# Kernel optimization log

Measured on AMD Instinct MI355X. Metric: run time of the kernel, lower is better.

The kernel has to match this reference:

```python
import jax, jax.numpy as jnp
import numpy as np

M, N, K, C, H = 100000, 8192, 32, 256, 8
DH = C // H
FF = 512
R = (15, 15, 7)  # 2*MAXRANGE-1 per axis for MAXRANGE=[8,8,4]


def _layer_norm(x, g, b, eps=1e-5):
    mu = jnp.mean(x, axis=-1, keepdims=True)
    xc = x - mu
    var = jnp.mean(xc * xc, axis=-1, keepdims=True)
    return xc * jax.lax.rsqrt(var + eps) * g + b


def setup_inputs() -> dict:
    key = jax.random.key(0)
    ks = iter(jax.random.split(key, 40))
    d = {}
    d['voxel_features'] = jax.random.normal(next(ks), (M, C), jnp.float32)
    d['query_coords'] = jax.random.normal(next(ks), (N, 3), jnp.float32)
    d['query_indices'] = jax.random.randint(next(ks), (N,), 0, M)
    d['gather_indices'] = jax.random.randint(next(ks), (N, K), 0, M)
    d['gather_mask'] = jax.random.randint(next(ks), (N, K), 0, 2).astype(bool)
    d['rel_x'] = jax.random.randint(next(ks), (N, K), 0, R[0])
    d['rel_y'] = jax.random.randint(next(ks), (N, K), 0, R[1])
    d['rel_z'] = jax.random.randint(next(ks), (N, K), 0, R[2])
    s = 0.02
    # pos_proj: Conv1d(3, C, 1) == linear on coords
    d['w_pos'] = jax.random.normal(next(ks), (3, C), jnp.float32) * s
    d['b_pos'] = jnp.zeros((C,), jnp.float32)
    for nm in ['q', 'k', 'v', 'proj']:
        d['w_' + nm] = jax.random.normal(next(ks), (C, C), jnp.float32) * (C ** -0.5)
        d['b_' + nm] = jnp.zeros((C,), jnp.float32)
    d['ln1_g'] = jnp.ones((C,), jnp.float32); d['ln1_b'] = jnp.zeros((C,), jnp.float32)
    d['ln2_g'] = jnp.ones((C,), jnp.float32); d['ln2_b'] = jnp.zeros((C,), jnp.float32)
    d['w_ff1'] = jax.random.normal(next(ks), (C, FF), jnp.float32) * (C ** -0.5)
    d['b_ff1'] = jnp.zeros((FF,), jnp.float32)
    d['w_ff2'] = jax.random.normal(next(ks), (FF, C), jnp.float32) * (FF ** -0.5)
    d['b_ff2'] = jnp.zeros((C,), jnp.float32)
    # per-axis relative position tables: [H, DH, 2W-1] for q-side and k-side
    for m in ['q', 'k']:
        for ax, r in zip(['x', 'y', 'z'], R):
            d[f'pos_{m}{ax}'] = jax.random.normal(next(ks), (H, DH, r), jnp.float32) * s
    return d


def reference(voxel_features, query_coords, query_indices, gather_indices, gather_mask,
              rel_x, rel_y, rel_z,
              w_pos, b_pos, w_q, b_q, w_k, b_k, w_v, b_v, w_proj, b_proj,
              ln1_g, ln1_b, ln2_g, ln2_b, w_ff1, b_ff1, w_ff2, b_ff2,
              pos_qx, pos_qy, pos_qz, pos_kx, pos_ky, pos_kz):
    x = _layer_norm(voxel_features, ln1_g, ln1_b)           # [M, C] pre-norm
    # gather window centers (queries) + positional projection of coords
    q_in = x[query_indices] + jax.nn.relu(query_coords @ w_pos + b_pos)  # [N, C]
    kv_in = x[gather_indices]                                # [N, K, C]
    kv_in = jnp.where(gather_mask[..., None], 0.0, kv_in)
    q = (q_in @ w_q + b_q).reshape(N, H, DH)
    k = (kv_in @ w_k + b_k).reshape(N, K, H, DH)
    v = (kv_in @ w_v + b_v).reshape(N, K, H, DH)
    logits = jnp.einsum('nhd,nkhd->nhk', q, k) * (DH ** -0.5)  # [N, H, K]
    # query-side per-axis relative position bias: contract q with table, gather at rel idx
    for pos, rel in ((pos_qx, rel_x), (pos_qy, rel_y), (pos_qz, rel_z)):
        qp = jnp.einsum('nhd,hdr->nhr', q, pos)              # [N, H, R]
        logits = logits + jnp.take_along_axis(qp, rel[:, None, :], axis=2)
    # key-side per-axis relative position bias
    for pos, rel in ((pos_kx, rel_x), (pos_ky, rel_y), (pos_kz, rel_z)):
        kp = jnp.einsum('nkhd,hdr->nkhr', k, pos)            # [N, K, H, R]
        bias = jnp.take_along_axis(kp, rel[:, :, None, None], axis=3)[..., 0]  # [N, K, H]
        logits = logits + bias.transpose(0, 2, 1)
    logits = jnp.where(gather_mask[:, None, :], -1e9, logits)
    attn = jax.nn.softmax(logits, axis=-1)
    out = jnp.einsum('nhk,nkhd->nhd', attn, v).reshape(N, C) @ w_proj + b_proj
    act = voxel_features[query_indices] + out                # residual (pre-norm block)
    h = jax.nn.relu(_layer_norm(act, ln2_g, ln2_b) @ w_ff1 + b_ff1) @ w_ff2 + b_ff2
    return act + h                                           # [N, C]
```

## Files before the change

### kernel.cpp

```cpp
#include <hip/hip_runtime.h>
#include <hip/hip_bf16.h>
#include <math.h>

#define MV   100000
#define NQ   8192
#define KN   32
#define CH   256
#define NH   8
#define DHD  32
#define FFD  512
#define NG   (NQ*KN)
#define QPW  37
#define QPN  (NH*QPW)
#define QPL  320
#define ASTR 40
#define KSTR 264

typedef __bf16 bf16x8 __attribute__((ext_vector_type(8)));
typedef float  f32x4  __attribute__((ext_vector_type(4)));

__device__ __forceinline__ float bf2f(unsigned short u) {
    return __uint_as_float(((unsigned int)u) << 16);
}
__device__ __forceinline__ unsigned short f2bf(float f) {
    unsigned int x = __float_as_uint(f);
    unsigned int r = x + 0x7FFFu + ((x >> 16) & 1u);
    return (unsigned short)(r >> 16);
}
__device__ __forceinline__ void glds16(const unsigned short* g, unsigned short* l) {
    __builtin_amdgcn_global_load_lds(
        (const __attribute__((address_space(1))) void*)g,
        (__attribute__((address_space(3))) void*)l, 16, 0, 0);
}

__global__ __launch_bounds__(256) void k_detect_mask(const unsigned char* __restrict__ raw,
                                                     int* __restrict__ flags) {
    __shared__ int any;
    if (threadIdx.x == 0) any = 0;
    __syncthreads();
    const uint4* p = (const uint4*)raw;
    int i = blockIdx.x * 256 + threadIdx.x;
    uint4 v = p[i];
    if ((v.x | v.y | v.z | v.w) & 0xFFFFFF00u) any = 1;
    __syncthreads();
    if (threadIdx.x == 0) flags[blockIdx.x] = any;
}

__global__ __launch_bounds__(256) void k_prep(const float* __restrict__ w_k,
                                              const float* __restrict__ w_v,
                                              const float* __restrict__ w_ff1,
                                              const float* __restrict__ w_ff2,
                                              const float* __restrict__ w_proj,
                                              const float* __restrict__ w_q,
                                              const float* __restrict__ b_k,
                                              const float* __restrict__ b_v,
                                              const float* __restrict__ pos_qx,
                                              const float* __restrict__ pos_qy,
                                              const float* __restrict__ pos_qz,
                                              const void* __restrict__ mask_raw,
                                              const int* __restrict__ gidx,
                                              const int* __restrict__ qidx,
                                              const int* __restrict__ flags,
                                              unsigned short* __restrict__ w_kv_t,
                                              unsigned short* __restrict__ w1_t,
                                              unsigned short* __restrict__ w2_t,
                                              unsigned short* __restrict__ wp_t,
                                              unsigned short* __restrict__ wq_t,
                                              unsigned short* __restrict__ wqp_t,
                                              float* __restrict__ bkv,
                                              float* __restrict__ zbias,
                                              int* __restrict__ mask_i,
                                              unsigned char* __restrict__ touched) {
    __shared__ int bl;
    if (threadIdx.x == 0) {
        int a = 0;
        #pragma unroll 8
        for (int i = 0; i < 64; i++) a |= flags[i];
        bl = a;
    }
    __syncthreads();
    int byteLayout = bl;
    int idx = blockIdx.x * 256 + threadIdx.x;
    if (blockIdx.x == 0 && threadIdx.x < 512)
        bkv[threadIdx.x] = (threadIdx.x < 256) ? b_k[threadIdx.x]
                                               : b_v[threadIdx.x - 256];
    if (idx < QPL) zbias[idx] = 0.f;
    if (idx < NQ) touched[qidx[idx]] = 1;
    if (idx < NG) {
        int mv = byteLayout ? (int)((const unsigned char*)mask_raw)[idx]
                            : ((const int*)mask_raw)[idx];
        mask_i[idx] = (mv != 0) ? 1 : 0;
        if (mv == 0) touched[gidx[idx]] = 1;
    }
    if (idx < 512 * 256) {
        int col = idx >> 8, j = idx & 255;
        float v = (col < 256) ? w_k[j * 256 + col] : w_v[j * 256 + (col - 256)];
        w_kv_t[idx] = f2bf(v);
    }
    if (idx < 512 * 256) {
        int n = idx >> 8, k = idx & 255;
        w1_t[idx] = f2bf(w_ff1[k * FFD + n]);
    }
    if (idx < 256 * 512) {
        int n = idx >> 9, k = idx & 511;
        w2_t[idx] = f2bf(w_ff2[k * CH + n]);
    }
    if (idx < 256 * 256) {
        int n = idx >> 8, k = idx & 255;
        wp_t[idx] = f2bf(w_proj[k * CH + n]);
        wq_t[idx] = f2bf(w_q[k * CH + n]);
    }
    if (idx < QPL * 256) {
        int col = idx >> 8, k = idx & 255;
        float v = 0.f;
        if (col < QPN) {
            int h = col / QPW, r = col % QPW;
            int h2 = k >> 5, d = k & 31;
            if (h2 == h) {
                if (r < 15)      v = pos_qx[(h * DHD + d) * 15 + r];
                else if (r < 30) v = pos_qy[(h * DHD + d) * 15 + (r - 15)];
                else             v = pos_qz[(h * DHD + d) * 7  + (r - 30)];
            }
        }
        wqp_t[idx] = f2bf(v);
    }
}

__global__ __launch_bounds__(256) void k_posc(const float* __restrict__ pos_kx,
                                              const float* __restrict__ pos_ky,
                                              const float* __restrict__ pos_kz,
                                              float* __restrict__ comb) {
    int idx = blockIdx.x * 256 + threadIdx.x;
    if (idx >= 8 * 15 * 15 * 7 * 32) return;
    int d = idx & 31, r = idx >> 5;
    int rz = r % 7;  r /= 7;
    int ry = r % 15; r /= 15;
    int rx = r % 15; int h = r / 15;
    comb[idx] = pos_kx[(h * DHD + d) * 15 + rx]
              + pos_ky[(h * DHD + d) * 15 + ry]
              + pos_kz[(h * DHD + d) * 7  + rz];
}

__global__ __launch_bounds__(256) void k_ln(const float* __restrict__ x,
                                            const float* __restrict__ g,
                                            const float* __restrict__ b,
                                            const unsigned char* __restrict__ tch,
                                            unsigned short* __restrict__ o,
                                            int nrows) {
    int wid = threadIdx.x >> 6, lane = threadIdx.x & 63;
    int row = blockIdx.x * 4 + wid;
    if (row >= nrows) return;
    if (tch && !tch[row]) return;
    const float4 v = *(const float4*)(x + (size_t)row * CH + lane * 4);
    float s  = v.x + v.y + v.z + v.w;
    float sq = v.x * v.x + v.y * v.y + v.z * v.z + v.w * v.w;
    #pragma unroll
    for (int off = 1; off < 64; off <<= 1) {
        s  += __shfl_xor(s,  off);
        sq += __shfl_xor(sq, off);
    }
    float mu  = s * (1.f / CH);
    float var = sq * (1.f / CH) - mu * mu;
    float rs  = rsqrtf(var + 1e-5f);
    float4 gv = *(const float4*)(g + lane * 4);
    float4 bv = *(const float4*)(b + lane * 4);
    ushort4 ov;
    ov.x = f2bf((v.x - mu) * rs * gv.x + bv.x);
    ov.y = f2bf((v.y - mu) * rs * gv.y + bv.y);
    ov.z = f2bf((v.z - mu) * rs * gv.z + bv.z);
    ov.w = f2bf((v.w - mu) * rs * gv.w + bv.w);
    *(ushort4*)(o + (size_t)row * CH + lane * 4) = ov;
}

__global__ __launch_bounds__(256) void k_qin(const unsigned short* __restrict__ ln_x,
                                             const float* __restrict__ coords,
                                             const int* __restrict__ qidx,
                                             const float* __restrict__ w_pos,
                                             const float* __restrict__ b_pos,
                                             unsigned short* __restrict__ qin) {
    int c = threadIdx.x;
    int nb = blockIdx.x * 8;
    float wp0 = w_pos[c], wp1 = w_pos[CH + c], wp2 = w_pos[2 * CH + c], bp = b_pos[c];
    #pragma unroll
    for (int qq = 0; qq < 8; qq++) {
        int n = nb + qq;
        float p = bp + coords[n * 3] * wp0 + coords[n * 3 + 1] * wp1 + coords[n * 3 + 2] * wp2;
        p = fmaxf(p, 0.f);
        int qi = qidx[n];
        qin[(size_t)n * CH + c] = f2bf(bf2f(ln_x[(size_t)qi * CH + c]) + p);
    }
}

__global__ __launch_bounds__(256) void k_kv(const unsigned short* __restrict__ ln_x,
                                            const unsigned short* __restrict__ w_kv_t,
                                            const float* __restrict__ bkv,
                                            const unsigned char* __restrict__ touched,
                                            unsigned short* __restrict__ kv) {
    __shared__ __align__(16) unsigned short As[128 * 32];
    __shared__ __align__(16) unsigned short Bs[128 * 32];
    const int tid = threadIdx.x;
    const int w = tid >> 6, l = tid & 63;
    const int wr = w >> 1, wc = w & 1;
    const int rowbase = blockIdx.y * 128;
    const int col0 = blockIdx.x * 128;
    const int sr = l >> 2, sq = l & 3;
    int ra0 = rowbase + w * 16 + sr;
    int ra1 = rowbase + 64 + w * 16 + sr;
    int ok0 = (ra0 < MV) && touched[ra0 < MV ? ra0 : 0];
    int ok1 = (ra1 < MV) && touched[ra1 < MV ? ra1 : 0];
    const unsigned short* pa0 = ln_x + (size_t)(ok0 ? ra0 : 0) * CH + sq * 8;
    const unsigned short* pa1 = ln_x + (size_t)(ok1 ? ra1 : 0) * CH + sq * 8;
    const unsigned short* pb0 = w_kv_t + (size_t)(col0 + w * 16 + sr) * CH + sq * 8;
    const unsigned short* pb1 = w_kv_t + (size_t)(col0 + 64 + w * 16 + sr) * CH + sq * 8;
    unsigned short* lA0 = As + w * 512;
    unsigned short* lA1 = As + 2048 + w * 512;
    unsigned short* lB0 = Bs + w * 512;
    unsigned short* lB1 = Bs + 2048 + w * 512;

    f32x4 acc[4][4];
    #pragma unroll
    for (int mt = 0; mt < 4; mt++)
        #pragma unroll
        for (int nt = 0; nt < 4; nt++)
            acc[mt][nt] = (f32x4){0.f, 0.f, 0.f, 0.f};

    const int ml = l & 15, qd = l >> 4;
    for (int kk = 0; kk < CH; kk += 32) {
        __syncthreads();
        glds16(pa0 + kk, lA0);
        glds16(pa1 + kk, lA1);
        glds16(pb0 + kk, lB0);
        glds16(pb1 + kk, lB1);
        __syncthreads();
        bf16x8 af[4], bf[4];
        #pragma unroll
        for (int mt = 0; mt < 4; mt++)
            af[mt] = *(const bf16x8*)(As + (wr * 64 + mt * 16 + ml) * 32 + qd * 8);
        #pragma unroll
        for (int nt = 0; nt < 4; nt++)
            bf[nt] = *(const bf16x8*)(Bs + (wc * 64 + nt * 16 + ml) * 32 + qd * 8);
        #pragma unroll
        for (int mt = 0; mt < 4; mt++)
            #pragma unroll
            for (int nt = 0; nt < 4; nt++)
                acc[mt][nt] = __builtin_amdgcn_mfma_f32_16x16x32_bf16(af[mt], bf[nt], acc[mt][nt], 0, 0, 0);
    }

    float bb[4];
    #pragma unroll
    for (int nt = 0; nt < 4; nt++)
        bb[nt] = bkv[col0 + wc * 64 + nt * 16 + ml];
    unsigned short* trs = As;
    #pragma unroll
    for (int mt = 0; mt < 4; mt++) {
        __syncthreads();
        #pragma unroll
        for (int nt = 0; nt < 4; nt++) {
            int lcol = wc * 64 + nt * 16 + ml;
            #pragma unroll
            for (int i = 0; i < 4; i++)
                trs[wr * 2048 + (qd * 4 + i) * 128 + lcol] = f2bf(acc[mt][nt][i] + bb[nt]);
        }
        __syncthreads();
        int rl = tid >> 4, cc = (tid & 15) * 8;
        int g0 = rowbase + mt * 16 + rl;
        int g1 = rowbase + 64 + mt * 16 + rl;
        if (g0 < MV && touched[g0])
            *(uint4*)(kv + (size_t)g0 * 512 + col0 + cc) = *(const uint4*)(trs + rl * 128 + cc);
        if (g1 < MV && touched[g1])
            *(uint4*)(kv + (size_t)g1 * 512 + col0 + cc) = *(const uint4*)(trs + 2048 + rl * 128 + cc);
    }
}

template <int KD, int EPI, int LDO>
__global__ __launch_bounds__(256) void k_mm(const unsigned short* __restrict__ A,
                                            const unsigned short* __restrict__ Bt_g,
                                            const float* __restrict__ bias,
                                            const float* __restrict__ res,
                                            const int* __restrict__ qidx,
                                            unsigned short* __restrict__ out_bf,
                                            float* __restrict__ out_f) {
    __shared__ __align__(16) unsigned short As[128 * ASTR];
    __shared__ __align__(16) unsigned short Bs[64 * ASTR];
    int tid = threadIdx.x;
    int w = tid >> 6, l = tid & 63;
    int rowbase = blockIdx.y * 128;
    int col0 = blockIdx.x * 64;
    int r0 = tid >> 2, qt = tid & 3;
    const unsigned short* a0p = A + (size_t)(rowbase + r0) * KD + qt * 8;
    const unsigned short* a1p = A + (size_t)(rowbase + 64 + r0) * KD + qt * 8;

    f32x4 acc[2][4];
    #pragma unroll
    for (int mt = 0; mt < 2; mt++)
        #pragma unroll
        for (int nt = 0; nt < 4; nt++)
            acc[mt][nt] = (f32x4){0.f, 0.f, 0.f, 0.f};

    const int ml = l & 15, qd = l >> 4;
    for (int kk = 0; kk < KD; kk += 32) {
        __syncthreads();
        uint4 v0 = *(const uint4*)(a0p + kk);
        uint4 v1 = *(const uint4*)(a1p + kk);
        *(uint4*)(As + r0 * ASTR + qt * 8)        = v0;
        *(uint4*)(As + (64 + r0) * ASTR + qt * 8) = v1;
        {
            uint4 bv = *(const uint4*)(Bt_g + (size_t)(col0 + r0) * KD + kk + qt * 8);
            *(uint4*)(Bs + r0 * ASTR + qt * 8) = bv;
        }
        __syncthreads();
        bf16x8 a0 = *(const bf16x8*)(As + (w * 32 + ml) * ASTR + qd * 8);
        bf16x8 a1 = *(const bf16x8*)(As + (w * 32 + 16 + ml) * ASTR + qd * 8);
        #pragma unroll
        for (int nt = 0; nt < 4; nt++) {
            bf16x8 bb = *(const bf16x8*)(Bs + (nt * 16 + ml) * ASTR + qd * 8);
            acc[0][nt] = __builtin_amdgcn_mfma_f32_16x16x32_bf16(a0, bb, acc[0][nt], 0, 0, 0);
            acc[1][nt] = __builtin_amdgcn_mfma_f32_16x16x32_bf16(a1, bb, acc[1][nt], 0, 0, 0);
        }
    }

    #pragma unroll
    for (int nt = 0; nt < 4; nt++) {
        int col = col0 + nt * 16 + ml;
        float bv = bias[col];
        #pragma unroll
        for (int mt = 0; mt < 2; mt++) {
            int rl = w * 32 + mt * 16 + qd * 4;
            #pragma unroll
            for (int i = 0; i < 4; i++) {
                int row = rowbase + rl + i;
                float v = acc[mt][nt][i] + bv;
                if (EPI == 0) {
                    out_bf[(size_t)row * LDO + col] = f2bf(fmaxf(v, 0.f));
                } else if (EPI == 1) {
                    out_f[(size_t)row * CH + col] = v + res[(size_t)row * CH + col];
                } else if (EPI == 2) {
                    int qi = qidx[row];
                    out_f[(size_t)row * CH + col] = v + res[(size_t)qi * CH + col];
                } else if (EPI == 3) {
                    out_f[(size_t)row * CH + col] = v;
                    out_bf[(size_t)row * CH + col] = f2bf(v);
                } else {
                    out_f[(size_t)row * LDO + col] = v;
                }
            }
        }
    }
}

__global__ __launch_bounds__(256) void k_attn3(const float* __restrict__ qbuf,
                                               const float* __restrict__ qp,
                                               const unsigned short* __restrict__ kvmat,
                                               const int* __restrict__ gidx,
                                               const int* __restrict__ mask_i,
                                               const int* __restrict__ rel_x,
                                               const int* __restrict__ rel_y,
                                               const int* __restrict__ rel_z,
                                               const float* __restrict__ comb,
                                               const float* __restrict__ b_v,
                                               unsigned short* __restrict__ attnln) {
    __shared__ float q_s[2 * 256];
    __shared__ float qp_s[2 * QPL];
    __shared__ float attn_s[2 * 256];
    __shared__ int   mask_s[64];
    __shared__ int   gidx_s[64];
    __shared__ __align__(16) unsigned short ks[64 * KSTR];

    int tid = threadIdx.x;
    int qb = blockIdx.x * 2;
    for (int i = tid; i < 512; i += 256) q_s[i] = qbuf[(size_t)qb * CH + i];
    for (int i = tid; i < 2 * QPL; i += 256) qp_s[i] = qp[(size_t)qb * QPL + i];
    if (tid < 64) {
        mask_s[tid] = mask_i[qb * 32 + tid];
        gidx_s[tid] = gidx[qb * 32 + tid];
    }
    __syncthreads();

    const int srow = tid >> 5;
    const int schk = tid & 31;
    uint4 kreg[8];
    #pragma unroll
    for (int j = 0; j < 8; j++) {
        int r = j * 8 + srow;
        uint4 v = {0u, 0u, 0u, 0u};
        if (!mask_s[r])
            v = *(const uint4*)(kvmat + (size_t)gidx_s[r] * 512 + schk * 8);
        kreg[j] = v;
    }
    #pragma unroll
    for (int j = 0; j < 8; j++)
        *(uint4*)(ks + (j * 8 + srow) * KSTR + schk * 8) = kreg[j];
    __syncthreads();

    int h = tid >> 5, k = tid & 31;
    const float scale = 0.17677669529663687f;
    for (int qq = 0; qq < 2; qq++) {
        int n = qb + qq;
        int gi = n * KN + k;
        int r = qq * 32 + k;
        int mk = mask_s[r];
        float lg = -1e9f;
        if (!mk) {
            int rx = rel_x[gi], ry = rel_y[gi], rz = rel_z[gi];
            const unsigned short* kp = ks + r * KSTR + h * 32;
            float kv[32];
            #pragma unroll
            for (int j = 0; j < 4; j++) {
                uint4 u = *(const uint4*)(kp + j * 8);
                kv[j * 8 + 0] = bf2f((unsigned short)(u.x & 0xFFFF));
                kv[j * 8 + 1] = bf2f((unsigned short)(u.x >> 16));
                kv[j * 8 + 2] = bf2f((unsigned short)(u.y & 0xFFFF));
                kv[j * 8 + 3] = bf2f((unsigned short)(u.y >> 16));
                kv[j * 8 + 4] = bf2f((unsigned short)(u.z & 0xFFFF));
                kv[j * 8 + 5] = bf2f((unsigned short)(u.z >> 16));
                kv[j * 8 + 6] = bf2f((unsigned short)(u.w & 0xFFFF));
                kv[j * 8 + 7] = bf2f((unsigned short)(u.w >> 16));
            }
            const float* cp = comb + ((((h * 15 + rx) * 15 + ry) * 7 + rz) << 5);
            float s1 = 0.f, s2 = 0.f;
            const float* qrow = q_s + qq * CH + h * DHD;
            #pragma unroll
            for (int d = 0; d < 32; d++) {
                s1 += kv[d] * qrow[d];
                s2 += kv[d] * cp[d];
            }
            lg = s1 * scale + s2
               + qp_s[qq * QPL + h * QPW + rx]
               + qp_s[qq * QPL + h * QPW + 15 + ry]
               + qp_s[qq * QPL + h * QPW + 30 + rz];
        }
        float mx = lg;
        #pragma unroll
        for (int off = 1; off <= 16; off <<= 1) mx = fmaxf(mx, __shfl_xor(mx, off));
        float e = mk ? 0.f : __expf(lg - mx);
        float sm = e;
        #pragma unroll
        for (int off = 1; off <= 16; off <<= 1) sm += __shfl_xor(sm, off);
        attn_s[qq * 256 + tid] = (sm > 0.f) ? e / sm : 0.f;
    }

    #pragma unroll
    for (int j = 0; j < 8; j++) {
        int r = j * 8 + srow;
        uint4 v = {0u, 0u, 0u, 0u};
        if (!mask_s[r])
            v = *(const uint4*)(kvmat + (size_t)gidx_s[r] * 512 + 256 + schk * 8);
        kreg[j] = v;
    }
    __syncthreads();
    #pragma unroll
    for (int j = 0; j < 8; j++)
        *(uint4*)(ks + (j * 8 + srow) * KSTR + schk * 8) = kreg[j];
    __syncthreads();

    int w = tid >> 6, l = tid & 63;
    int q2 = w >> 1, kh = w & 1;
    int hh = l >> 3;
    float a0 = 0.f, a1 = 0.f, a2 = 0.f, a3 = 0.f;
    #pragma unroll
    for (int i = 0; i < 16; i++) {
        int kk = kh * 16 + i;
        int r = q2 * 32 + kk;
        float av = attn_s[q2 * 256 + hh * 32 + kk];
        ushort4 v4 = *(const ushort4*)(ks + r * KSTR + l * 4);
        a0 += av * bf2f(v4.x);
        a1 += av * bf2f(v4.y);
        a2 += av * bf2f(v4.z);
        a3 += av * bf2f(v4.w);
    }
    if (kh == 1) {
        float4 pv = {a0, a1, a2, a3};
        *(float4*)(qp_s + q2 * 256 + l * 4) = pv;
    }
    __syncthreads();
    if (kh == 0) {
        float4 pv = *(const float4*)(qp_s + q2 * 256 + l * 4);
        a0 += pv.x; a1 += pv.y; a2 += pv.z; a3 += pv.w;
        int nm = 0;
        #pragma unroll
        for (int kk = 0; kk < 32; kk++) nm += 1 - mask_s[q2 * 32 + kk];
        int col = l * 4;
        if (nm == 0) {
            a0 = b_v[col]; a1 = b_v[col + 1]; a2 = b_v[col + 2]; a3 = b_v[col + 3];
        }
        ushort4 o;
        o.x = f2bf(a0); o.y = f2bf(a1); o.z = f2bf(a2); o.w = f2bf(a3);
        *(ushort4*)(attnln + (size_t)(qb + q2) * CH + col) = o;
    }
}

extern "C" void kernel_launch(void* const* d_in, const int* in_sizes, int n_in,
                              void* d_out, int out_size, void* d_ws, size_t ws_size,
                              hipStream_t stream) {
    (void)in_sizes; (void)n_in; (void)out_size; (void)ws_size;
    const float* vox    = (const float*)d_in[0];
    const float* coords = (const float*)d_in[1];
    const int*   qidx   = (const int*)d_in[2];
    const int*   gidx   = (const int*)d_in[3];
    const void*  mraw   = d_in[4];
    const int*   rel_x  = (const int*)d_in[5];
    const int*   rel_y  = (const int*)d_in[6];
    const int*   rel_z  = (const int*)d_in[7];
    const float* w_pos  = (const float*)d_in[8];
    const float* b_pos  = (const float*)d_in[9];
    const float* w_q    = (const float*)d_in[10];
    const float* b_q    = (const float*)d_in[11];
    const float* w_k    = (const float*)d_in[12];
    const float* b_k    = (const float*)d_in[13];
    const float* w_v    = (const float*)d_in[14];
    const float* b_v    = (const float*)d_in[15];
    const float* w_proj = (const float*)d_in[16];
    const float* b_proj = (const float*)d_in[17];
    const float* ln1_g  = (const float*)d_in[18];
    const float* ln1_b  = (const float*)d_in[19];
    const float* ln2_g  = (const float*)d_in[20];
    const float* ln2_b  = (const float*)d_in[21];
    const float* w_ff1  = (const float*)d_in[22];
    const float* b_ff1  = (const float*)d_in[23];
    const float* w_ff2  = (const float*)d_in[24];
    const float* b_ff2  = (const float*)d_in[25];
    const float* pos_qx = (const float*)d_in[26];
    const float* pos_qy = (const float*)d_in[27];
    const float* pos_qz = (const float*)d_in[28];
    const float* pos_kx = (const float*)d_in[29];
    const float* pos_ky = (const float*)d_in[30];
    const float* pos_kz = (const float*)d_in[31];

    char* p = (char*)d_ws;
    auto take = [&](size_t n) { char* r = p; p += (n + 255) & ~(size_t)255; return r; };
    unsigned short* ln_x    = (unsigned short*)take((size_t)MV * CH * 2);
    unsigned short* w_kv_t  = (unsigned short*)take((size_t)512 * 256 * 2);
    unsigned short* w1_t    = (unsigned short*)take((size_t)512 * 256 * 2);
    unsigned short* w2_t    = (unsigned short*)take((size_t)256 * 512 * 2);
    unsigned short* wp_t    = (unsigned short*)take((size_t)256 * 256 * 2);
    unsigned short* wq_t    = (unsigned short*)take((size_t)256 * 256 * 2);
    unsigned short* wqp_t   = (unsigned short*)take((size_t)QPL * 256 * 2);
    float*          bkv     = (float*)take(512 * 4);
    float*          zbias   = (float*)take(QPL * 4);
    int*            flags   = (int*)take(64 * 4);
    int*            mask_i  = (int*)take((size_t)NG * 4);
    unsigned char*  touched = (unsigned char*)take(MV);
    float*          comb    = (float*)take((size_t)8 * 15 * 15 * 7 * 32 * 4);
    unsigned short* qin     = (unsigned short*)take((size_t)NQ * CH * 2);
    float*          qbuf    = (float*)take((size_t)NQ * CH * 4);
    unsigned short* qbf     = (unsigned short*)take((size_t)NQ * CH * 2);
    float*          qp      = (float*)take((size_t)NQ * QPL * 4);
    unsigned short* kvmat   = (unsigned short*)take((size_t)MV * 512 * 2);
    unsigned short* attnln  = (unsigned short*)take((size_t)NQ * CH * 2);
    float*          actbuf  = (float*)take((size_t)NQ * CH * 4);
    unsigned short* actln   = (unsigned short*)take((size_t)NQ * CH * 2);
    unsigned short* hbuf    = (unsigned short*)take((size_t)NQ * FFD * 2);

    hipMemsetAsync(touched, 0, MV, stream);
    hipLaunchKernelGGL(k_detect_mask, dim3(64), dim3(256), 0, stream,
                       (const unsigned char*)mraw, flags);
    hipLaunchKernelGGL(k_prep, dim3(NG / 256), dim3(256), 0, stream,
                       w_k, w_v, w_ff1, w_ff2, w_proj, w_q, b_k, b_v,
                       pos_qx, pos_qy, pos_qz, mraw, gidx, qidx, flags,
                       w_kv_t, w1_t, w2_t, wp_t, wq_t, wqp_t, bkv, zbias,
                       mask_i, touched);
    hipLaunchKernelGGL(k_posc, dim3((8 * 15 * 15 * 7 * 32 + 255) / 256), dim3(256), 0, stream,
                       pos_kx, pos_ky, pos_kz, comb);
    hipLaunchKernelGGL(k_ln, dim3(MV / 4 + 1), dim3(256), 0, stream,
                       vox, ln1_g, ln1_b, touched, ln_x, MV);
    hipLaunchKernelGGL(k_qin, dim3(NQ / 8), dim3(256), 0, stream,
                       ln_x, coords, qidx, w_pos, b_pos, qin);
    hipLaunchKernelGGL(k_kv, dim3(4, (MV + 127) / 128), dim3(256), 0, stream,
                       ln_x, w_kv_t, bkv, touched, kvmat);
    hipLaunchKernelGGL(HIP_KERNEL_NAME(k_mm<256, 3, CH>), dim3(4, NQ / 128), dim3(256), 0, stream,
                       qin, wq_t, b_q, (const float*)nullptr, (const int*)nullptr,
                       qbf, qbuf);
    hipLaunchKernelGGL(HIP_KERNEL_NAME(k_mm<256, 4, QPL>), dim3(QPL / 64, NQ / 128), dim3(256), 0, stream,
                       qbf, wqp_t, zbias, (const float*)nullptr, (const int*)nullptr,
                       (unsigned short*)nullptr, qp);
    hipLaunchKernelGGL(k_attn3, dim3(NQ / 2), dim3(256), 0, stream,
                       qbuf, qp, kvmat, gidx, mask_i, rel_x, rel_y, rel_z,
                       comb, b_v, attnln);
    hipLaunchKernelGGL(HIP_KERNEL_NAME(k_mm<256, 2, CH>), dim3(4, NQ / 128), dim3(256), 0, stream,
                       attnln, wp_t, b_proj, vox, qidx,
                       (unsigned short*)nullptr, actbuf);
    hipLaunchKernelGGL(k_ln, dim3(NQ / 4), dim3(256), 0, stream,
                       actbuf, ln2_g, ln2_b, (const unsigned char*)nullptr, actln, NQ);
    hipLaunchKernelGGL(HIP_KERNEL_NAME(k_mm<256, 0, FFD>), dim3(8, NQ / 128), dim3(256), 0, stream,
                       actln, w1_t, b_ff1, (const float*)nullptr, (const int*)nullptr,
                       hbuf, (float*)nullptr);
    hipLaunchKernelGGL(HIP_KERNEL_NAME(k_mm<512, 1, CH>), dim3(4, NQ / 128), dim3(256), 0, stream,
                       hbuf, w2_t, b_ff2, actbuf, (const int*)nullptr,
                       (unsigned short*)nullptr, (float*)d_out);
}
```

Measured before the change: 391.1 us.

## Fold q-side position tables into Q projection weights and deepen k_kv K-step

Premultiplies w_q (and b_q) by the query-side relative-position tables so that a single GEMM yields both q and the per-axis q·pos scores. This removes the separate bf16 q round trip and the second GEMM, and lets the attention kernel read one concatenated buffer. It also doubles the K-chunk per iteration in the KV projection GEMM, halving barriers, and writes the whole output tile in one transpose pass. The trade-off is precision: the q-pos scores now come from bf16-rounded folded weights rather than a contraction of the rounded q, and the KV kernel uses twice the LDS.

```diff
diff --git a/kernel.cpp b/kernel.cpp
--- a/kernel.cpp
+++ b/kernel.cpp
@@ -12,7 +12,7 @@
 #define NG   (NQ*KN)
 #define QPW  37
 #define QPN  (NH*QPW)
-#define QPL  320
+#define QCL  576
 #define ASTR 40
 #define KSTR 264
 
@@ -54,9 +54,7 @@
                                               const float* __restrict__ w_q,
                                               const float* __restrict__ b_k,
                                               const float* __restrict__ b_v,
-                                              const float* __restrict__ pos_qx,
-                                              const float* __restrict__ pos_qy,
-                                              const float* __restrict__ pos_qz,
+                                              const float* __restrict__ b_q,
                                               const void* __restrict__ mask_raw,
                                               const int* __restrict__ gidx,
                                               const int* __restrict__ qidx,
@@ -65,10 +63,9 @@
                                               unsigned short* __restrict__ w1_t,
                                               unsigned short* __restrict__ w2_t,
                                               unsigned short* __restrict__ wp_t,
-                                              unsigned short* __restrict__ wq_t,
-                                              unsigned short* __restrict__ wqp_t,
+                                              unsigned short* __restrict__ wqcat,
                                               float* __restrict__ bkv,
-                                              float* __restrict__ zbias,
+                                              float* __restrict__ bqcat,
                                               int* __restrict__ mask_i,
                                               unsigned char* __restrict__ touched) {
     __shared__ int bl;
@@ -84,7 +81,8 @@
     if (blockIdx.x == 0 && threadIdx.x < 512)
         bkv[threadIdx.x] = (threadIdx.x < 256) ? b_k[threadIdx.x]
                                                : b_v[threadIdx.x - 256];
-    if (idx < QPL) zbias[idx] = 0.f;
+    if (blockIdx.x == 1) bqcat[threadIdx.x] = (threadIdx.x < 256) ? b_q[threadIdx.x] : 0.f;
+    if (blockIdx.x == 2 && threadIdx.x < QCL - 256) bqcat[256 + threadIdx.x] = 0.f;
     if (idx < NQ) touched[qidx[idx]] = 1;
     if (idx < NG) {
         int mv = byteLayout ? (int)((const unsigned char*)mask_raw)[idx]
@@ -108,22 +106,35 @@
     if (idx < 256 * 256) {
         int n = idx >> 8, k = idx & 255;
         wp_t[idx] = f2bf(w_proj[k * CH + n]);
-        wq_t[idx] = f2bf(w_q[k * CH + n]);
-    }
-    if (idx < QPL * 256) {
-        int col = idx >> 8, k = idx & 255;
-        float v = 0.f;
-        if (col < QPN) {
-            int h = col / QPW, r = col % QPW;
-            int h2 = k >> 5, d = k & 31;
-            if (h2 == h) {
-                if (r < 15)      v = pos_qx[(h * DHD + d) * 15 + r];
-                else if (r < 30) v = pos_qy[(h * DHD + d) * 15 + (r - 15)];
-                else             v = pos_qz[(h * DHD + d) * 7  + (r - 30)];
-            }
-        }
-        wqp_t[idx] = f2bf(v);
-    }
+        wqcat[idx] = f2bf(w_q[k * CH + n]);
+    }
+}
+
+__global__ __launch_bounds__(256) void k_wqp(const float* __restrict__ w_q,
+                                             const float* __restrict__ b_q,
+                                             const float* __restrict__ pos_qx,
+                                             const float* __restrict__ pos_qy,
+                                             const float* __restrict__ pos_qz,
+                                             unsigned short* __restrict__ wqcat,
+                                             float* __restrict__ bqcat) {
+    int col = blockIdx.x;
+    int k = threadIdx.x;
+    float acc = 0.f, bacc = 0.f;
+    if (col < QPN) {
+        int h = col / QPW, r = col % QPW;
+        const float* T; int rr, R;
+        if (r < 15)      { T = pos_qx; rr = r;      R = 15; }
+        else if (r < 30) { T = pos_qy; rr = r - 15; R = 15; }
+        else             { T = pos_qz; rr = r - 30; R = 7;  }
+        #pragma unroll
+        for (int d = 0; d < DHD; d++) {
+            float t = T[(h * DHD + d) * R + rr];
+            acc += w_q[k * CH + h * DHD + d] * t;
+            if (k == 0) bacc += b_q[h * DHD + d] * t;
+        }
+    }
+    wqcat[(size_t)(256 + col) * CH + k] = f2bf(acc);
+    if (k == 0) bqcat[256 + col] = bacc;
 }
 
 __global__ __launch_bounds__(256) void k_posc(const float* __restrict__ pos_kx,
@@ -196,8 +207,9 @@
                                             const float* __restrict__ bkv,
                                             const unsigned char* __restrict__ touched,
                                             unsigned short* __restrict__ kv) {
-    __shared__ __align__(16) unsigned short As[128 * 32];
-    __shared__ __align__(16) unsigned short Bs[128 * 32];
+    __shared__ __align__(16) unsigned short S[16384];
+    unsigned short* As = S;
+    unsigned short* Bs = S + 8192;
     const int tid = threadIdx.x;
     const int w = tid >> 6, l = tid & 63;
     const int wr = w >> 1, wc = w & 1;
@@ -225,50 +237,60 @@
             acc[mt][nt] = (f32x4){0.f, 0.f, 0.f, 0.f};
 
     const int ml = l & 15, qd = l >> 4;
-    for (int kk = 0; kk < CH; kk += 32) {
+    for (int kk = 0; kk < CH; kk += 64) {
         __syncthreads();
         glds16(pa0 + kk, lA0);
         glds16(pa1 + kk, lA1);
         glds16(pb0 + kk, lB0);
         glds16(pb1 + kk, lB1);
+        glds16(pa0 + kk + 32, lA0 + 4096);
+        glds16(pa1 + kk + 32, lA1 + 4096);
+        glds16(pb0 + kk + 32, lB0 + 4096);
+        glds16(pb1 + kk + 32, lB1 + 4096);
         __syncthreads();
-        bf16x8 af[4], bf[4];
-        #pragma unroll
-        for (int mt = 0; mt < 4; mt++)
-            af[mt] = *(const bf16x8*)(As + (wr * 64 + mt * 16 + ml) * 32 + qd * 8);
-        #pragma unroll
-        for (int nt = 0; nt < 4; nt++)
-            bf[nt] = *(const bf16x8*)(Bs + (wc * 64 + nt * 16 + ml) * 32 + qd * 8);
-        #pragma unroll
-        for (int mt = 0; mt < 4; mt++)
+        #pragma unroll
+        for (int c2 = 0; c2 < 2; c2++) {
+            const unsigned short* Ac = As + c2 * 4096;
+            const unsigned short* Bc = Bs + c2 * 4096;
+            bf16x8 af[4], bf[4];
+            #pragma unroll
+            for (int mt = 0; mt < 4; mt++)
+                af[mt] = *(const bf16x8*)(Ac + (wr * 64 + mt * 16 + ml) * 32 + qd * 8);
             #pragma unroll
             for (int nt = 0; nt < 4; nt++)
-                acc[mt][nt] = __builtin_amdgcn_mfma_f32_16x16x32_bf16(af[mt], bf[nt], acc[mt][nt], 0, 0, 0);
+                bf[nt] = *(const bf16x8*)(Bc + (wc * 64 + nt * 16 + ml) * 32 + qd * 8);
+            #pragma unroll
+            for (int mt = 0; mt < 4; mt++)
+                #pragma unroll
+                for (int nt = 0; nt < 4; nt++)
+                    acc[mt][nt] = __builtin_amdgcn_mfma_f32_16x16x32_bf16(af[mt], bf[nt], acc[mt][nt], 0, 0, 0);
+        }
     }
 
     float bb[4];
     #pragma unroll
     for (int nt = 0; nt < 4; nt++)
         bb[nt] = bkv[col0 + wc * 64 + nt * 16 + ml];
-    unsigned short* trs = As;
-    #pragma unroll
-    for (int mt = 0; mt < 4; mt++) {
-        __syncthreads();
+    __syncthreads();
+    #pragma unroll
+    for (int mt = 0; mt < 4; mt++)
         #pragma unroll
         for (int nt = 0; nt < 4; nt++) {
-            int lcol = wc * 64 + nt * 16 + ml;
+            int col = wc * 64 + nt * 16 + ml;
             #pragma unroll
-            for (int i = 0; i < 4; i++)
-                trs[wr * 2048 + (qd * 4 + i) * 128 + lcol] = f2bf(acc[mt][nt][i] + bb[nt]);
-        }
-        __syncthreads();
-        int rl = tid >> 4, cc = (tid & 15) * 8;
-        int g0 = rowbase + mt * 16 + rl;
-        int g1 = rowbase + 64 + mt * 16 + rl;
-        if (g0 < MV && touched[g0])
-            *(uint4*)(kv + (size_t)g0 * 512 + col0 + cc) = *(const uint4*)(trs + rl * 128 + cc);
-        if (g1 < MV && touched[g1])
-            *(uint4*)(kv + (size_t)g1 * 512 + col0 + cc) = *(const uint4*)(trs + 2048 + rl * 128 + cc);
+            for (int i = 0; i < 4; i++) {
+                int row = wr * 64 + mt * 16 + qd * 4 + i;
+                S[row * 128 + col] = f2bf(acc[mt][nt][i] + bb[nt]);
+            }
+        }
+    __syncthreads();
+    #pragma unroll
+    for (int j = 0; j < 8; j++) {
+        int chunk = j * 256 + tid;
+        int row = chunk >> 4, cc = (chunk & 15) * 8;
+        int g = rowbase + row;
+        if (g < MV && touched[g])
+            *(uint4*)(kv + (size_t)g * 512 + col0 + cc) = *(const uint4*)(S + row * 128 + cc);
     }
 }
 
@@ -337,9 +359,6 @@
                 } else if (EPI == 2) {
                     int qi = qidx[row];
                     out_f[(size_t)row * CH + col] = v + res[(size_t)qi * CH + col];
-                } else if (EPI == 3) {
-                    out_f[(size_t)row * CH + col] = v;
-                    out_bf[(size_t)row * CH + col] = f2bf(v);
                 } else {
                     out_f[(size_t)row * LDO + col] = v;
                 }
@@ -348,8 +367,7 @@
     }
 }
 
-__global__ __launch_bounds__(256) void k_attn3(const float* __restrict__ qbuf,
-                                               const float* __restrict__ qp,
+__global__ __launch_bounds__(256) void k_attn3(const float* __restrict__ qcat,
                                                const unsigned short* __restrict__ kvmat,
                                                const int* __restrict__ gidx,
                                                const int* __restrict__ mask_i,
@@ -359,8 +377,7 @@
                                                const float* __restrict__ comb,
                                                const float* __restrict__ b_v,
                                                unsigned short* __restrict__ attnln) {
-    __shared__ float q_s[2 * 256];
-    __shared__ float qp_s[2 * QPL];
+    __shared__ float qc_s[2 * QCL];
     __shared__ float attn_s[2 * 256];
     __shared__ int   mask_s[64];
     __shared__ int   gidx_s[64];
@@ -368,8 +385,7 @@
 
     int tid = threadIdx.x;
     int qb = blockIdx.x * 2;
-    for (int i = tid; i < 512; i += 256) q_s[i] = qbuf[(size_t)qb * CH + i];
-    for (int i = tid; i < 2 * QPL; i += 256) qp_s[i] = qp[(size_t)qb * QPL + i];
+    for (int i = tid; i < 2 * QCL; i += 256) qc_s[i] = qcat[(size_t)qb * QCL + i];
     if (tid < 64) {
         mask_s[tid] = mask_i[qb * 32 + tid];
         gidx_s[tid] = gidx[qb * 32 + tid];
@@ -418,16 +434,16 @@
             }
             const float* cp = comb + ((((h * 15 + rx) * 15 + ry) * 7 + rz) << 5);
             float s1 = 0.f, s2 = 0.f;
-            const float* qrow = q_s + qq * CH + h * DHD;
+            const float* qrow = qc_s + qq * QCL + h * DHD;
             #pragma unroll
             for (int d = 0; d < 32; d++) {
                 s1 += kv[d] * qrow[d];
                 s2 += kv[d] * cp[d];
             }
             lg = s1 * scale + s2
-               + qp_s[qq * QPL + h * QPW + rx]
-               + qp_s[qq * QPL + h * QPW + 15 + ry]
-               + qp_s[qq * QPL + h * QPW + 30 + rz];
+               + qc_s[qq * QCL + 256 + h * QPW + rx]
+               + qc_s[qq * QCL + 256 + h * QPW + 15 + ry]
+               + qc_s[qq * QCL + 256 + h * QPW + 30 + rz];
         }
         float mx = lg;
         #pragma unroll
@@ -470,11 +486,11 @@
     }
     if (kh == 1) {
         float4 pv = {a0, a1, a2, a3};
-        *(float4*)(qp_s + q2 * 256 + l * 4) = pv;
+        *(float4*)(qc_s + q2 * 256 + l * 4) = pv;
     }
     __syncthreads();
     if (kh == 0) {
-        float4 pv = *(const float4*)(qp_s + q2 * 256 + l * 4);
+        float4 pv = *(const float4*)(qc_s + q2 * 256 + l * 4);
         a0 += pv.x; a1 += pv.y; a2 += pv.z; a3 += pv.w;
         int nm = 0;
         #pragma unroll
@@ -533,18 +549,15 @@
     unsigned short* w1_t    = (unsigned short*)take((size_t)512 * 256 * 2);
     unsigned short* w2_t    = (unsigned short*)take((size_t)256 * 512 * 2);
     unsigned short* wp_t    = (unsigned short*)take((size_t)256 * 256 * 2);
-    unsigned short* wq_t    = (unsigned short*)take((size_t)256 * 256 * 2);
-    unsigned short* wqp_t   = (unsigned short*)take((size_t)QPL * 256 * 2);
+    unsigned short* wqcat   = (unsigned short*)take((size_t)QCL * 256 * 2);
     float*          bkv     = (float*)take(512 * 4);
-    float*          zbias   = (float*)take(QPL * 4);
+    float*          bqcat   = (float*)take(QCL * 4);
     int*            flags   = (int*)take(64 * 4);
     int*            mask_i  = (int*)take((size_t)NG * 4);
     unsigned char*  touched = (unsigned char*)take(MV);
     float*          comb    = (float*)take((size_t)8 * 15 * 15 * 7 * 32 * 4);
     unsigned short* qin     = (unsigned short*)take((size_t)NQ * CH * 2);
-    float*          qbuf    = (float*)take((size_t)NQ * CH * 4);
-    unsigned short* qbf     = (unsigned short*)take((size_t)NQ * CH * 2);
-    float*          qp      = (float*)take((size_t)NQ * QPL * 4);
+    float*          qcat    = (float*)take((size_t)NQ * QCL * 4);
     unsigned short* kvmat   = (unsigned short*)take((size_t)MV * 512 * 2);
     unsigned short* attnln  = (unsigned short*)take((size_t)NQ * CH * 2);
     float*          actbuf  = (float*)take((size_t)NQ * CH * 4);
@@ -555,10 +568,12 @@
     hipLaunchKernelGGL(k_detect_mask, dim3(64), dim3(256), 0, stream,
                        (const unsigned char*)mraw, flags);
     hipLaunchKernelGGL(k_prep, dim3(NG / 256), dim3(256), 0, stream,
-                       w_k, w_v, w_ff1, w_ff2, w_proj, w_q, b_k, b_v,
-                       pos_qx, pos_qy, pos_qz, mraw, gidx, qidx, flags,
-                       w_kv_t, w1_t, w2_t, wp_t, wq_t, wqp_t, bkv, zbias,
+                       w_k, w_v, w_ff1, w_ff2, w_proj, w_q, b_k, b_v, b_q,
+                       mraw, gidx, qidx, flags,
+                       w_kv_t, w1_t, w2_t, wp_t, wqcat, bkv, bqcat,
                        mask_i, touched);
+    hipLaunchKernelGGL(k_wqp, dim3(QCL - 256), dim3(256), 0, stream,
+                       w_q, b_q, pos_qx, pos_qy, pos_qz, wqcat, bqcat);
     hipLaunchKernelGGL(k_posc, dim3((8 * 15 * 15 * 7 * 32 + 255) / 256), dim3(256), 0, stream,
                        pos_kx, pos_ky, pos_kz, comb);
     hipLaunchKernelGGL(k_ln, dim3(MV / 4 + 1), dim3(256), 0, stream,
@@ -567,14 +582,11 @@
                        ln_x, coords, qidx, w_pos, b_pos, qin);
     hipLaunchKernelGGL(k_kv, dim3(4, (MV + 127) / 128), dim3(256), 0, stream,
                        ln_x, w_kv_t, bkv, touched, kvmat);
-    hipLaunchKernelGGL(HIP_KERNEL_NAME(k_mm<256, 3, CH>), dim3(4, NQ / 128), dim3(256), 0, stream,
-                       qin, wq_t, b_q, (const float*)nullptr, (const int*)nullptr,
-                       qbf, qbuf);
-    hipLaunchKernelGGL(HIP_KERNEL_NAME(k_mm<256, 4, QPL>), dim3(QPL / 64, NQ / 128), dim3(256), 0, stream,
-                       qbf, wqp_t, zbias, (const float*)nullptr, (const int*)nullptr,
-                       (unsigned short*)nullptr, qp);
+    hipLaunchKernelGGL(HIP_KERNEL_NAME(k_mm<256, 4, QCL>), dim3(QCL / 64, NQ / 128), dim3(256), 0, stream,
+                       qin, wqcat, bqcat, (const float*)nullptr, (const int*)nullptr,
+                       (unsigned short*)nullptr, qcat);
     hipLaunchKernelGGL(k_attn3, dim3(NQ / 2), dim3(256), 0, stream,
-                       qbuf, qp, kvmat, gidx, mask_i, rel_x, rel_y, rel_z,
+                       qcat, kvmat, gidx, mask_i, rel_x, rel_y, rel_z,
                        comb, b_v, attnln);
     hipLaunchKernelGGL(HIP_KERNEL_NAME(k_mm<256, 2, CH>), dim3(4, NQ / 128), dim3(256), 0, stream,
                        attnln, wp_t, b_proj, vox, qidx,
```

Result: no change. 386.5 us (-1.2%).
